# Kernel optimization log

Measured on AMD Instinct MI355X. Metric: run time of the kernel, lower is better.

The kernel has to match this reference:

```python
import jax, jax.numpy as jnp
import numpy as np

V, E, H, S, B = 50000, 1024, 1024, 512, 64  # vocab, emb(=input_size), hidden, seq_len, batch


def setup_inputs() -> dict:
    key = jax.random.key(0)
    ks = jax.random.split(key, 11)
    s = 0.05
    return {
        "input_tensor": jax.random.randint(ks[0], (B, S), 0, V),
        "target_idx": jax.random.randint(ks[1], (B,), 0, S),
        "emb": jax.random.normal(ks[2], (V, E), jnp.float32) * s,
        # per-direction stacked weights; layer0 input = E, layer1 input = 2H
        "w_ih_l0": jax.random.normal(ks[3], (2, 4 * H, E), jnp.float32) * s,
        "w_hh_l0": jax.random.normal(ks[4], (2, 4 * H, H), jnp.float32) * s,
        "b_l0": jax.random.normal(ks[5], (2, 4 * H), jnp.float32) * s,  # b_ih + b_hh folded
        "w_ih_l1": jax.random.normal(ks[6], (2, 4 * H, 2 * H), jnp.float32) * s,
        "w_hh_l1": jax.random.normal(ks[7], (2, 4 * H, H), jnp.float32) * s,
        "b_l1": jax.random.normal(ks[8], (2, 4 * H), jnp.float32) * s,
        "w_cls": jax.random.normal(ks[9], (1, 2 * H), jnp.float32) * s,
        "b_cls": jax.random.normal(ks[10], (1,), jnp.float32) * s,
    }


def _lstm_dir(xs, w_ih, w_hh, b):
    # xs: [S, B, in] ; forward-in-time scan (torch code steps the BiLSTM one
    # timestep at a time, so BOTH directions effectively run forward in time).
    xw = jnp.einsum('sbi,gi->sbg', xs, w_ih) + b  # [S, B, 4H]
    h0 = jnp.zeros((xs.shape[1], w_hh.shape[1]), xs.dtype)

    def step(carry, xt):
        h, c = carry
        gates = xt + h @ w_hh.T
        i, f, g, o = jnp.split(gates, 4, axis=-1)  # torch gate order i,f,g,o
        c = jax.nn.sigmoid(f) * c + jax.nn.sigmoid(i) * jnp.tanh(g)
        h = jax.nn.sigmoid(o) * jnp.tanh(c)
        return (h, c), h

    _, hs = jax.lax.scan(step, (h0, h0), xw)
    return hs  # [S, B, H]


def _bilstm_layer(xs, w_ih, w_hh, b):
    hs = jax.vmap(_lstm_dir, in_axes=(None, 0, 0, 0))(xs, w_ih, w_hh, b)  # [2,S,B,H]
    return jnp.concatenate([hs[0], hs[1]], axis=-1)  # [S, B, 2H]


def reference(input_tensor, target_idx, emb, w_ih_l0, w_hh_l0, b_l0,
              w_ih_l1, w_hh_l1, b_l1, w_cls, b_cls):
    bsz = input_tensor.shape[0]
    x = emb[input_tensor]                      # [B, S, E]
    x = jnp.transpose(x, (1, 0, 2))            # [S, B, E] (seq-major, as torch LSTM)
    y = _bilstm_layer(x, w_ih_l0, w_hh_l0, b_l0)
    y = _bilstm_layer(y, w_ih_l1, w_hh_l1, b_l1)  # [S, B, 2H]
    tgt = y[target_idx, jnp.arange(bsz)]       # gather hidden at target position: [B, 2H]
    logits = tgt @ w_cls.T + b_cls             # [B, 1]
    return jax.nn.sigmoid(logits).reshape(bsz)
```

## Files before the change

kernel.cpp:

```cpp
#include <hip/hip_runtime.h>
#include <stdint.h>

#define SLEN 512
#define NBATCH 64
#define EMB 1024
#define HID 1024
#define G4 4096
#define D2H 2048
#define CT 64
#define NC (SLEN/CT)
#define CROWS (CT*NBATCH)
#define HSLOT (NBATCH*D2H)

typedef __bf16 bf16x8 __attribute__((ext_vector_type(8)));
typedef float  f32x4  __attribute__((ext_vector_type(4)));

__device__ __forceinline__ ushort f2bf(float x){
  union { float f; uint32_t u; } v; v.f = x;
  uint32_t r = (v.u + 0x7fffu + ((v.u >> 16) & 1u)) >> 16;
  return (ushort)r;
}
__device__ __forceinline__ float bf2f(uint32_t u){
  union { uint32_t u; float f; } v; v.u = u << 16;
  return v.f;
}
__device__ __forceinline__ float sigm(float x){ return 1.f / (1.f + __expf(-x)); }
__device__ __forceinline__ float tanh_s(float x){ return 2.f / (1.f + __expf(-2.f*x)) - 1.f; }

__device__ __forceinline__ void async_ld16(const ushort* g, ushort* l){
  __builtin_amdgcn_global_load_lds(
      (const __attribute__((address_space(1))) uint32_t*)g,
      (__attribute__((address_space(3))) uint32_t*)l, 16, 0, 0);
}

__global__ void k_zero(uint32_t* p, int n){
  int i = blockIdx.x * 256 + threadIdx.x;
  if (i < n) p[i] = 0;
}

__global__ void k_convert(const float4* __restrict__ src, ushort4* __restrict__ dst, int n4){
  int i = blockIdx.x * blockDim.x + threadIdx.x;
  if (i < n4){
    float4 v = src[i];
    ushort4 o; o.x = f2bf(v.x); o.y = f2bf(v.y); o.z = f2bf(v.z); o.w = f2bf(v.w);
    dst[i] = o;
  }
}

__global__ void k_gather_c(const int* __restrict__ inp, const float* __restrict__ emb,
                           ushort* __restrict__ xbf, int tbase){
  int row = blockIdx.x;
  int s = tbase + (row >> 6), b = row & 63;
  int t = threadIdx.x;
  int v = inp[b * SLEN + s];
  float4 x = ((const float4*)(emb + (size_t)v * EMB))[t];
  ushort4 o; o.x = f2bf(x.x); o.y = f2bf(x.y); o.z = f2bf(x.z); o.w = f2bf(x.w);
  ((ushort4*)(xbf + (size_t)row * EMB))[t] = o;
}

__global__ __launch_bounds__(256) void k_gemm(const ushort* __restrict__ A,
                                              const ushort* __restrict__ Bw,
                                              const float* __restrict__ bias,
                                              ushort* __restrict__ C, int K,
                                              size_t cDirStride){
  __shared__ __align__(16) ushort sA[128 * 32];
  __shared__ __align__(16) ushort sB[128 * 32];
  const int tid = threadIdx.x;
  const int d = blockIdx.z;
  const size_t mBase = (size_t)blockIdx.x * 128;
  const int nBase = blockIdx.y * 128;
  const ushort* Bd = Bw + (size_t)d * G4 * K;
  const float* biasd = bias + (size_t)d * G4;
  ushort* Cd = C + (size_t)d * cDirStride;
  const int w = tid >> 6, lane = tid & 63;
  const int quad = lane >> 4, c16 = lane & 15;
  const int m0 = (w >> 1) * 64, n0 = (w & 1) * 64;
  const int u0 = tid, u1 = tid + 256;
  const int r0 = u0 >> 2, k0 = (u0 & 3) * 8;
  const int r1 = u1 >> 2, k1 = (u1 & 3) * 8;

  f32x4 acc[4][4] = {};
  for (int kc = 0; kc < K; kc += 32){
    __syncthreads();
    async_ld16(A  + (mBase + r0) * (size_t)K + kc + k0, sA + u0 * 8);
    async_ld16(A  + (mBase + r1) * (size_t)K + kc + k1, sA + u1 * 8);
    async_ld16(Bd + (size_t)(nBase + r0) * K + kc + k0, sB + u0 * 8);
    async_ld16(Bd + (size_t)(nBase + r1) * K + kc + k1, sB + u1 * 8);
    __syncthreads();
    bf16x8 af[4], bfv[4];
#pragma unroll
    for (int mt = 0; mt < 4; ++mt)
      af[mt] = *(const bf16x8*)(sA + (m0 + mt * 16 + c16) * 32 + quad * 8);
#pragma unroll
    for (int nt = 0; nt < 4; ++nt)
      bfv[nt] = *(const bf16x8*)(sB + (n0 + nt * 16 + c16) * 32 + quad * 8);
#pragma unroll
    for (int mt = 0; mt < 4; ++mt)
#pragma unroll
      for (int nt = 0; nt < 4; ++nt)
        acc[mt][nt] = __builtin_amdgcn_mfma_f32_16x16x32_bf16(af[mt], bfv[nt], acc[mt][nt], 0, 0, 0);
  }
#pragma unroll
  for (int nt = 0; nt < 4; ++nt){
    int col = nBase + n0 + nt * 16 + c16;
    float bv = biasd[col];
#pragma unroll
    for (int mt = 0; mt < 4; ++mt){
      size_t rowb = mBase + m0 + mt * 16 + quad * 4;
#pragma unroll
      for (int r = 0; r < 4; ++r)
        Cd[(rowb + r) * G4 + col] = f2bf(acc[mt][nt][r] + bv);
    }
  }
}

__global__ __launch_bounds__(256, 2) void k_rec(const ushort* __restrict__ xw0,
                                                const ushort* __restrict__ xw1,
                                                const ushort* __restrict__ whh0,
                                                const ushort* __restrict__ whh1,
                                                const ushort* __restrict__ hinit0,
                                                const ushort* __restrict__ hinit1,
                                                ushort* __restrict__ h0seq,
                                                ushort* __restrict__ h1seq,
                                                float* __restrict__ c0st,
                                                float* __restrict__ c1st,
                                                unsigned* __restrict__ flags,
                                                int act, int tbase0, int tbase1,
                                                unsigned tok0, unsigned tok1,
                                                const int* __restrict__ tgt_idx,
                                                float* __restrict__ tgt_out){
  const int layer = blockIdx.x >> 8;
  if (!((act >> layer) & 1)) return;
  const int bx = blockIdx.x & 255;

  const ushort* xw    = layer ? xw1    : xw0;
  const ushort* whh   = layer ? whh1   : whh0;
  const ushort* hinit = layer ? hinit1 : hinit0;
  ushort* hseq        = layer ? h1seq  : h0seq;
  float* cst          = layer ? c1st   : c0st;
  const int mode      = layer;
  const int tbase     = layer ? tbase1 : tbase0;
  const unsigned tok  = layer ? tok1 : tok0;

  const int tid = threadIdx.x;
  const int d  = bx >> 7;
  const int jt = (bx & 127) >> 1;
  const int mh = bx & 1;
  const int j0 = jt * 16;
  const int mb = mh * 32;
  const int w = tid >> 6, lane = tid & 63;
  const int quad = lane >> 4, c16 = lane & 15;
  const int g = w;
  const int er = tid >> 3;
  const int ec = (tid & 7) * 2;

  unsigned* fgrp = flags + (size_t)(((layer * 2 + d) * 2 + mh) * CT) * 64;

  __shared__ __align__(16) ushort hS[32 * 1024];
  __shared__ float sred[4 * 32 * 17];

  bf16x8 bfr[32];
  {
    const ushort* wp = whh + ((size_t)d * G4 + (size_t)g * HID + j0 + c16) * HID + quad * 8;
#pragma unroll
    for (int t = 0; t < 32; ++t) bfr[t] = *(const bf16x8*)(wp + t * 32);
  }

  float cv0 = cst[(size_t)bx * 512 + tid * 2];
  float cv1 = cst[(size_t)bx * 512 + tid * 2 + 1];

  const int tgt_t = mode ? tgt_idx[mb + er] : -1;

  const int stColU = (tid * 8) & 1023;
  const int stRB   = tid >> 7;

  const int swz = (c16 & 7) << 3;
  const ushort* bA = hS + c16 * 1024;
  const ushort* bB = hS + (16 + c16) * 1024;

  {
    const ushort* hp = hinit + (size_t)mb * D2H + d * HID;
#pragma unroll
    for (int r = 0; r < 16; ++r){
      int row  = 2 * r + stRB;
      int soff = stColU ^ ((row & 7) << 3);
      async_ld16(hp + (size_t)row * D2H + soff, hS + tid * 8 + r * 2048);
    }
  }
  size_t xrow = ((size_t)d * CROWS + mb + er) * G4;
  uint32_t xq0 = *(const uint32_t*)(xw + xrow + 0 * HID + j0 + ec);
  uint32_t xq1 = *(const uint32_t*)(xw + xrow + 1 * HID + j0 + ec);
  uint32_t xq2 = *(const uint32_t*)(xw + xrow + 2 * HID + j0 + ec);
  uint32_t xq3 = *(const uint32_t*)(xw + xrow + 3 * HID + j0 + ec);

  for (int i = 0; i < CT; ++i){
    ushort* hout = hseq + (size_t)i * HSLOT;

    __builtin_amdgcn_s_waitcnt(0);
    __syncthreads();

    f32x4 acc0 = {}, acc1 = {};
#pragma unroll
    for (int t = 0; t < 32; ++t){
      int cidx = (t * 32 + quad * 8) ^ swz;
      bf16x8 a0 = *(const bf16x8*)(bA + cidx);
      bf16x8 a1 = *(const bf16x8*)(bB + cidx);
      acc0 = __builtin_amdgcn_mfma_f32_16x16x32_bf16(a0, bfr[t], acc0, 0, 0, 0);
      acc1 = __builtin_amdgcn_mfma_f32_16x16x32_bf16(a1, bfr[t], acc1, 0, 0, 0);
    }

#pragma unroll
    for (int r = 0; r < 4; ++r){
      sred[(g * 32 + quad * 4 + r) * 17 + c16]      = acc0[r];
      sred[(g * 32 + 16 + quad * 4 + r) * 17 + c16] = acc1[r];
    }
    __syncthreads();

    float i0 = sred[(0 * 32 + er) * 17 + ec]     + bf2f(xq0 & 0xffffu);
    float i1 = sred[(0 * 32 + er) * 17 + ec + 1] + bf2f(xq0 >> 16);
    float f0 = sred[(1 * 32 + er) * 17 + ec]     + bf2f(xq1 & 0xffffu);
    float f1 = sred[(1 * 32 + er) * 17 + ec + 1] + bf2f(xq1 >> 16);
    float g0 = sred[(2 * 32 + er) * 17 + ec]     + bf2f(xq2 & 0xffffu);
    float g1 = sred[(2 * 32 + er) * 17 + ec + 1] + bf2f(xq2 >> 16);
    float o0 = sred[(3 * 32 + er) * 17 + ec]     + bf2f(xq3 & 0xffffu);
    float o1 = sred[(3 * 32 + er) * 17 + ec + 1] + bf2f(xq3 >> 16);
    float c0 = sigm(f0) * cv0 + sigm(i0) * tanh_s(g0);
    float c1 = sigm(f1) * cv1 + sigm(i1) * tanh_s(g1);
    float h0 = sigm(o0) * tanh_s(c0);
    float h1 = sigm(o1) * tanh_s(c1);
    cv0 = c0; cv1 = c1;

    uint32_t hp2 = (uint32_t)f2bf(h0) | ((uint32_t)f2bf(h1) << 16);
    size_t hoff = (size_t)(mb + er) * D2H + d * HID + j0 + ec;
    __hip_atomic_store((uint32_t*)(hout + hoff), hp2, __ATOMIC_RELAXED, __HIP_MEMORY_SCOPE_AGENT);

    if (mode && tgt_t == tbase + i){
      tgt_out[hoff]     = h0;
      tgt_out[hoff + 1] = h1;
    }

    if (i != CT - 1){
      __atomic_signal_fence(__ATOMIC_SEQ_CST);
      __builtin_amdgcn_s_waitcnt(0);
      __syncthreads();
      if (tid == 0)
        __hip_atomic_store(fgrp + i * 64 + jt, tok, __ATOMIC_RELAXED, __HIP_MEMORY_SCOPE_AGENT);
      if (tid < 64){
        const unsigned* fq = fgrp + i * 64 + lane;
        while (true){
          unsigned v = __hip_atomic_load(fq, __ATOMIC_RELAXED, __HIP_MEMORY_SCOPE_AGENT);
          if (__all((int)(v >= tok))) break;
          __builtin_amdgcn_s_sleep(1);
        }
      }
      __syncthreads();
      asm volatile("" ::: "memory");
      {
        const ushort* hp3 = hseq + (size_t)i * HSLOT + (size_t)mb * D2H + d * HID;
#pragma unroll
        for (int r = 0; r < 16; ++r){
          int row  = 2 * r + stRB;
          int soff = stColU ^ ((row & 7) << 3);
          async_ld16(hp3 + (size_t)row * D2H + soff, hS + tid * 8 + r * 2048);
        }
      }
      xrow = ((size_t)d * CROWS + (size_t)(i + 1) * NBATCH + mb + er) * G4;
      xq0 = *(const uint32_t*)(xw + xrow + 0 * HID + j0 + ec);
      xq1 = *(const uint32_t*)(xw + xrow + 1 * HID + j0 + ec);
      xq2 = *(const uint32_t*)(xw + xrow + 2 * HID + j0 + ec);
      xq3 = *(const uint32_t*)(xw + xrow + 3 * HID + j0 + ec);
    }
  }

  cst[(size_t)bx * 512 + tid * 2]     = cv0;
  cst[(size_t)bx * 512 + tid * 2 + 1] = cv1;
}

__global__ __launch_bounds__(256) void k_final(const float* __restrict__ tgt,
                                               const float* __restrict__ wc,
                                               const float* __restrict__ bc,
                                               float* __restrict__ out){
  int b = blockIdx.x, tid = threadIdx.x;
  const float4* tv = (const float4*)(tgt + (size_t)b * D2H);
  const float4* wv = (const float4*)wc;
  float s = 0.f;
  for (int i = tid; i < D2H / 4; i += 256){
    float4 a = tv[i], ww = wv[i];
    s += a.x * ww.x + a.y * ww.y + a.z * ww.z + a.w * ww.w;
  }
  for (int off = 32; off; off >>= 1) s += __shfl_down(s, off, 64);
  __shared__ float red[4];
  if ((tid & 63) == 0) red[tid >> 6] = s;
  __syncthreads();
  if (tid == 0){
    float tot = red[0] + red[1] + red[2] + red[3] + bc[0];
    out[b] = 1.f / (1.f + __expf(-tot));
  }
}

extern "C" void kernel_launch(void* const* d_in, const int* in_sizes, int n_in,
                              void* d_out, int out_size, void* d_ws, size_t ws_size,
                              hipStream_t stream){
  (void)in_sizes; (void)n_in; (void)out_size;
  const int*   inp   = (const int*)  d_in[0];
  const int*   tgtix = (const int*)  d_in[1];
  const float* emb   = (const float*)d_in[2];
  const float* wih0  = (const float*)d_in[3];
  const float* whh0  = (const float*)d_in[4];
  const float* bl0   = (const float*)d_in[5];
  const float* wih1  = (const float*)d_in[6];
  const float* whh1  = (const float*)d_in[7];
  const float* bl1   = (const float*)d_in[8];
  const float* wcls  = (const float*)d_in[9];
  const float* bcls  = (const float*)d_in[10];
  float* out = (float*)d_out;

  char* p = (char*)d_ws;
  ushort* wih0b = (ushort*)p; p += (size_t)2 * G4 * 1024 * 2;
  ushort* whh0b = (ushort*)p; p += (size_t)2 * G4 * 1024 * 2;
  ushort* wih1b = (ushort*)p; p += (size_t)2 * G4 * 2048 * 2;
  ushort* whh1b = (ushort*)p; p += (size_t)2 * G4 * 1024 * 2;
  ushort* xbf   = (ushort*)p; p += (size_t)CROWS * EMB * 2;
  ushort* xw0   = (ushort*)p; p += (size_t)2 * CROWS * G4 * 2;
  ushort* h0seq = (ushort*)p; p += (size_t)CT * HSLOT * 2;
  ushort* h1seq = (ushort*)p; p += (size_t)CT * HSLOT * 2;
  char* zbase = p;
  ushort* h0zero = (ushort*)p; p += (size_t)HSLOT * 2;
  float*  c0st   = (float*)p;  p += (size_t)256 * 512 * 4;
  float*  c1st   = (float*)p;  p += (size_t)256 * 512 * 4;
  unsigned* flags = (unsigned*)p; p += (size_t)2 * 4 * CT * 64 * 4;
  size_t zbytes = (size_t)(p - zbase);
  float* tgtb = (float*)p; p += (size_t)NBATCH * D2H * 4;

  const size_t xwBytes = (size_t)2 * CROWS * G4 * 2;
  bool pipe = ((size_t)(p - (char*)d_ws) + xwBytes) <= ws_size;
  ushort* xw1 = pipe ? (ushort*)p : xw0;

  int zn = (int)(zbytes / 4);
  k_zero<<<dim3((zn + 255) / 256), 256, 0, stream>>>((uint32_t*)zbase, zn);
  k_convert<<<dim3(8192),  256, 0, stream>>>((const float4*)wih0, (ushort4*)wih0b, 2 * G4 * 1024 / 4);
  k_convert<<<dim3(8192),  256, 0, stream>>>((const float4*)whh0, (ushort4*)whh0b, 2 * G4 * 1024 / 4);
  k_convert<<<dim3(16384), 256, 0, stream>>>((const float4*)wih1, (ushort4*)wih1b, 2 * G4 * 2048 / 4);
  k_convert<<<dim3(8192),  256, 0, stream>>>((const float4*)whh1, (ushort4*)whh1b, 2 * G4 * 1024 / 4);

  const size_t cds = (size_t)CROWS * G4;

  if (pipe){
    for (int t = 0; t <= NC; ++t){
      if (t < NC){
        k_gather_c<<<dim3(CROWS), 256, 0, stream>>>(inp, emb, xbf, t * CT);
        k_gemm<<<dim3(CROWS / 128, G4 / 128, 2), 256, 0, stream>>>(xbf, wih0b, bl0, xw0, EMB, cds);
      }
      if (t >= 1)
        k_gemm<<<dim3(CROWS / 128, G4 / 128, 2), 256, 0, stream>>>(h0seq, wih1b, bl1, xw1, D2H, cds);
      int act = (t < NC ? 1 : 0) | (t >= 1 ? 2 : 0);
      k_rec<<<dim3(512), 256, 0, stream>>>(xw0, xw1, whh0b, whh1b,
          (t == 0) ? h0zero : h0seq + (size_t)(CT - 1) * HSLOT,
          (t <= 1) ? h0zero : h1seq + (size_t)(CT - 1) * HSLOT,
          h0seq, h1seq, c0st, c1st, flags, act,
          t * CT, (t - 1) * CT,
          (unsigned)(t + 1), (unsigned)t,
          tgtix, tgtb);
    }
  } else {
    for (int c = 0; c < NC; ++c){
      int tbase = c * CT;
      k_gather_c<<<dim3(CROWS), 256, 0, stream>>>(inp, emb, xbf, tbase);
      k_gemm<<<dim3(CROWS / 128, G4 / 128, 2), 256, 0, stream>>>(xbf, wih0b, bl0, xw0, EMB, cds);
      k_rec<<<dim3(512), 256, 0, stream>>>(xw0, xw1, whh0b, whh1b,
          (c == 0) ? h0zero : h0seq + (size_t)(CT - 1) * HSLOT, h0zero,
          h0seq, h1seq, c0st, c1st, flags, 1,
          tbase, 0, (unsigned)(c + 1), 0u, tgtix, tgtb);
      k_gemm<<<dim3(CROWS / 128, G4 / 128, 2), 256, 0, stream>>>(h0seq, wih1b, bl1, xw1, D2H, cds);
      k_rec<<<dim3(512), 256, 0, stream>>>(xw0, xw1, whh0b, whh1b,
          h0zero, (c == 0) ? h0zero : h1seq + (size_t)(CT - 1) * HSLOT,
          h0seq, h1seq, c0st, c1st, flags, 2,
          0, tbase, 0u, (unsigned)(c + 1), tgtix, tgtb);
    }
  }

  k_final<<<dim3(NBATCH), 256, 0, stream>>>(tgtb, wcls, bcls, out);
}
```

Baseline: 7.151 ms.

## Interleave block mapping, split K across waves, and use per-thread flag polling

Blocks are now indexed so the layer, direction and batch half come from the low bits of the block id, which interleaves the groups across the grid. Each wave now computes two gates over half of K instead of one gate over all of K, and the two halves are combined through a two-phase shared-memory accumulation that adds one extra barrier per step. The cross-block wait is changed: each thread polls only the four producer flags for the column tile it will load, which removes the post-spin block barrier. The next step's input-projection loads are also issued before the spin so their latency overlaps the wait. The risks are the extra barrier in the reduction and more flag-polling traffic from every thread.

```diff
diff --git a/kernel.cpp b/kernel.cpp
--- a/kernel.cpp
+++ b/kernel.cpp
@@ -129,9 +129,14 @@
                                                 unsigned tok0, unsigned tok1,
                                                 const int* __restrict__ tgt_idx,
                                                 float* __restrict__ tgt_out){
-  const int layer = blockIdx.x >> 8;
+  const int bxp   = blockIdx.x;
+  const int grp   = bxp & 7;
+  const int layer = grp >> 2;
   if (!((act >> layer) & 1)) return;
-  const int bx = blockIdx.x & 255;
+  const int d  = (grp >> 1) & 1;
+  const int mh = grp & 1;
+  const int jt = bxp >> 3;
+  const int lb = jt * 4 + (d << 1) + mh;
 
   const ushort* xw    = layer ? xw1    : xw0;
   const ushort* whh   = layer ? whh1   : whh0;
@@ -143,14 +148,12 @@
   const unsigned tok  = layer ? tok1 : tok0;
 
   const int tid = threadIdx.x;
-  const int d  = bx >> 7;
-  const int jt = (bx & 127) >> 1;
-  const int mh = bx & 1;
   const int j0 = jt * 16;
   const int mb = mh * 32;
   const int w = tid >> 6, lane = tid & 63;
   const int quad = lane >> 4, c16 = lane & 15;
-  const int g = w;
+  const int gp = w & 1;
+  const int kh = w >> 1;
   const int er = tid >> 3;
   const int ec = (tid & 7) * 2;
 
@@ -159,20 +162,25 @@
   __shared__ __align__(16) ushort hS[32 * 1024];
   __shared__ float sred[4 * 32 * 17];
 
-  bf16x8 bfr[32];
+  bf16x8 bfr0[16], bfr1[16];
   {
-    const ushort* wp = whh + ((size_t)d * G4 + (size_t)g * HID + j0 + c16) * HID + quad * 8;
-#pragma unroll
-    for (int t = 0; t < 32; ++t) bfr[t] = *(const bf16x8*)(wp + t * 32);
-  }
-
-  float cv0 = cst[(size_t)bx * 512 + tid * 2];
-  float cv1 = cst[(size_t)bx * 512 + tid * 2 + 1];
+    const ushort* wpA = whh + ((size_t)d * G4 + (size_t)(gp * 2)     * HID + j0 + c16) * HID + quad * 8;
+    const ushort* wpB = whh + ((size_t)d * G4 + (size_t)(gp * 2 + 1) * HID + j0 + c16) * HID + quad * 8;
+#pragma unroll
+    for (int t = 0; t < 16; ++t){
+      bfr0[t] = *(const bf16x8*)(wpA + (kh * 16 + t) * 32);
+      bfr1[t] = *(const bf16x8*)(wpB + (kh * 16 + t) * 32);
+    }
+  }
+
+  float cv0 = cst[(size_t)lb * 512 + tid * 2];
+  float cv1 = cst[(size_t)lb * 512 + tid * 2 + 1];
 
   const int tgt_t = mode ? tgt_idx[mb + er] : -1;
 
   const int stColU = (tid * 8) & 1023;
   const int stRB   = tid >> 7;
+  const int myJtB  = (stColU >> 4) & ~3;
 
   const int swz = (c16 & 7) << 3;
   const ushort* bA = hS + c16 * 1024;
@@ -199,20 +207,37 @@
     __builtin_amdgcn_s_waitcnt(0);
     __syncthreads();
 
-    f32x4 acc0 = {}, acc1 = {};
-#pragma unroll
-    for (int t = 0; t < 32; ++t){
-      int cidx = (t * 32 + quad * 8) ^ swz;
+    f32x4 a00 = {}, a01 = {}, a10 = {}, a11 = {};
+#pragma unroll
+    for (int t = 0; t < 16; ++t){
+      int cidx = ((kh * 16 + t) * 32 + quad * 8) ^ swz;
       bf16x8 a0 = *(const bf16x8*)(bA + cidx);
       bf16x8 a1 = *(const bf16x8*)(bB + cidx);
-      acc0 = __builtin_amdgcn_mfma_f32_16x16x32_bf16(a0, bfr[t], acc0, 0, 0, 0);
-      acc1 = __builtin_amdgcn_mfma_f32_16x16x32_bf16(a1, bfr[t], acc1, 0, 0, 0);
-    }
-
-#pragma unroll
-    for (int r = 0; r < 4; ++r){
-      sred[(g * 32 + quad * 4 + r) * 17 + c16]      = acc0[r];
-      sred[(g * 32 + 16 + quad * 4 + r) * 17 + c16] = acc1[r];
+      a00 = __builtin_amdgcn_mfma_f32_16x16x32_bf16(a0, bfr0[t], a00, 0, 0, 0);
+      a01 = __builtin_amdgcn_mfma_f32_16x16x32_bf16(a1, bfr0[t], a01, 0, 0, 0);
+      a10 = __builtin_amdgcn_mfma_f32_16x16x32_bf16(a0, bfr1[t], a10, 0, 0, 0);
+      a11 = __builtin_amdgcn_mfma_f32_16x16x32_bf16(a1, bfr1[t], a11, 0, 0, 0);
+    }
+
+    const int G0 = gp * 2, G1 = gp * 2 + 1;
+    if (kh == 1){
+#pragma unroll
+      for (int r = 0; r < 4; ++r){
+        sred[(G0 * 32 +      quad * 4 + r) * 17 + c16] = a00[r];
+        sred[(G0 * 32 + 16 + quad * 4 + r) * 17 + c16] = a01[r];
+        sred[(G1 * 32 +      quad * 4 + r) * 17 + c16] = a10[r];
+        sred[(G1 * 32 + 16 + quad * 4 + r) * 17 + c16] = a11[r];
+      }
+    }
+    __syncthreads();
+    if (kh == 0){
+#pragma unroll
+      for (int r = 0; r < 4; ++r){
+        sred[(G0 * 32 +      quad * 4 + r) * 17 + c16] += a00[r];
+        sred[(G0 * 32 + 16 + quad * 4 + r) * 17 + c16] += a01[r];
+        sred[(G1 * 32 +      quad * 4 + r) * 17 + c16] += a10[r];
+        sred[(G1 * 32 + 16 + quad * 4 + r) * 17 + c16] += a11[r];
+      }
     }
     __syncthreads();
 
@@ -245,15 +270,23 @@
       __syncthreads();
       if (tid == 0)
         __hip_atomic_store(fgrp + i * 64 + jt, tok, __ATOMIC_RELAXED, __HIP_MEMORY_SCOPE_AGENT);
-      if (tid < 64){
-        const unsigned* fq = fgrp + i * 64 + lane;
+      xrow = ((size_t)d * CROWS + (size_t)(i + 1) * NBATCH + mb + er) * G4;
+      xq0 = *(const uint32_t*)(xw + xrow + 0 * HID + j0 + ec);
+      xq1 = *(const uint32_t*)(xw + xrow + 1 * HID + j0 + ec);
+      xq2 = *(const uint32_t*)(xw + xrow + 2 * HID + j0 + ec);
+      xq3 = *(const uint32_t*)(xw + xrow + 3 * HID + j0 + ec);
+      {
+        const unsigned* fq = fgrp + i * 64 + myJtB;
         while (true){
-          unsigned v = __hip_atomic_load(fq, __ATOMIC_RELAXED, __HIP_MEMORY_SCOPE_AGENT);
-          if (__all((int)(v >= tok))) break;
+          unsigned v0 = __hip_atomic_load(fq + 0, __ATOMIC_RELAXED, __HIP_MEMORY_SCOPE_AGENT);
+          unsigned v1 = __hip_atomic_load(fq + 1, __ATOMIC_RELAXED, __HIP_MEMORY_SCOPE_AGENT);
+          unsigned v2 = __hip_atomic_load(fq + 2, __ATOMIC_RELAXED, __HIP_MEMORY_SCOPE_AGENT);
+          unsigned v3 = __hip_atomic_load(fq + 3, __ATOMIC_RELAXED, __HIP_MEMORY_SCOPE_AGENT);
+          bool ok = (v0 >= tok) & (v1 >= tok) & (v2 >= tok) & (v3 >= tok);
+          if (__all((int)ok)) break;
           __builtin_amdgcn_s_sleep(1);
         }
       }
-      __syncthreads();
       asm volatile("" ::: "memory");
       {
         const ushort* hp3 = hseq + (size_t)i * HSLOT + (size_t)mb * D2H + d * HID;
@@ -264,16 +297,11 @@
           async_ld16(hp3 + (size_t)row * D2H + soff, hS + tid * 8 + r * 2048);
         }
       }
-      xrow = ((size_t)d * CROWS + (size_t)(i + 1) * NBATCH + mb + er) * G4;
-      xq0 = *(const uint32_t*)(xw + xrow + 0 * HID + j0 + ec);
-      xq1 = *(const uint32_t*)(xw + xrow + 1 * HID + j0 + ec);
-      xq2 = *(const uint32_t*)(xw + xrow + 2 * HID + j0 + ec);
-      xq3 = *(const uint32_t*)(xw + xrow + 3 * HID + j0 + ec);
-    }
-  }
-
-  cst[(size_t)bx * 512 + tid * 2]     = cv0;
-  cst[(size_t)bx * 512 + tid * 2 + 1] = cv1;
+    }
+  }
+
+  cst[(size_t)lb * 512 + tid * 2]     = cv0;
+  cst[(size_t)lb * 512 + tid * 2 + 1] = cv1;
 }
 
 __global__ __launch_bounds__(256) void k_final(const float* __restrict__ tgt,
```

Result: slower. 8.955 ms (+25.2%).
